# Optimization experiments

Hardware: AMD Instinct MI355X
Metric: run time of the kernel (lower is better)

Reference implementation:

```python
import jax, jax.numpy as jnp
import numpy as np
from jax import lax

PAD_IDX = 0
SOS_IDX = 1


def gru_cell(x, h, w_ih, w_hh, b_ih, b_hh):
    # PyTorch GRU cell: gates ordered [r, z, n]
    gi = x @ w_ih.T + b_ih            # [B, 3H]
    gh = h @ w_hh.T + b_hh            # [B, 3H]
    i_r, i_z, i_n = jnp.split(gi, 3, axis=-1)
    h_r, h_z, h_n = jnp.split(gh, 3, axis=-1)
    r = jax.nn.sigmoid(i_r + h_r)
    z = jax.nn.sigmoid(i_z + h_z)
    n = jnp.tanh(i_n + r * h_n)
    return (1.0 - z) * n + z * h


def setup_inputs() -> dict:
    key = jax.random.key(0)
    ks = jax.random.split(key, 24)
    B, S, T = 32, 64, 48
    Vs, Vt, E, H = 32000, 32000, 512, 1024
    sH = 1.0 / np.sqrt(H)
    sE = 1.0 / np.sqrt(E)

    def p(k, shape, scale):
        return jax.random.normal(k, shape, jnp.float32) * scale

    inp = {
        'source_ids': jax.random.randint(ks[0], (B, S), 0, Vs),
        'target_ids': jax.random.randint(ks[1], (B, T), 0, Vt),
        'enc_embed': p(ks[2], (Vs, E), 0.02).at[PAD_IDX].set(0.0),
        'enc_w_ih': p(ks[3], (3 * H, E), sE),
        'enc_w_hh': p(ks[4], (3 * H, H), sH),
        'enc_b_ih': p(ks[5], (3 * H,), sH),
        'enc_b_hh': p(ks[6], (3 * H,), sH),
        'wq': p(ks[7], (H, H), sH),
        'bq': p(ks[8], (H,), sH),
        'wk': p(ks[9], (H, H), sH),
        'bk': p(ks[10], (H,), sH),
        'ws': p(ks[11], (H,), sH),
        'bs': p(ks[12], (), sH),
        'dec_embed': p(ks[13], (Vt, E), 0.02).at[PAD_IDX].set(0.0),
        'dec_w_ih': p(ks[14], (3 * H, E + H), sH),
        'dec_w_hh': p(ks[15], (3 * H, H), sH),
        'dec_b_ih': p(ks[16], (3 * H,), sH),
        'dec_b_hh': p(ks[17], (3 * H,), sH),
        'wo': p(ks[18], (Vt, H), sH),
        'bo': p(ks[19], (Vt,), sH),
    }
    return inp


def reference(source_ids, target_ids, enc_embed, enc_w_ih, enc_w_hh, enc_b_ih,
              enc_b_hh, wq, bq, wk, bk, ws, bs, dec_embed, dec_w_ih, dec_w_hh,
              dec_b_ih, dec_b_hh, wo, bo):
    B, S = source_ids.shape
    T = target_ids.shape[1]
    H = wq.shape[0]

    # ----- encoder GRU -----
    enc_emb = enc_embed[source_ids]                  # [B,S,E] (dropout = identity, eval)
    h0 = jnp.zeros((B, H), enc_emb.dtype)

    def enc_step(h, x):
        h = gru_cell(x, h, enc_w_ih, enc_w_hh, enc_b_ih, enc_b_hh)
        return h, h

    h_final, enc_out = lax.scan(enc_step, h0, enc_emb.transpose(1, 0, 2))
    enc_out = enc_out.transpose(1, 0, 2)             # [B,S,H]

    mask = source_ids != PAD_IDX                     # [B,S]
    keys_proj = enc_out @ wk.T + bk                  # [B,S,H] (hoisted; linear, step-invariant)

    # ----- decoder with teacher forcing (ratio=1.0 => always teacher) -----
    dec_in = jnp.concatenate(
        [jnp.full((B, 1), SOS_IDX, dtype=target_ids.dtype), target_ids[:, 1:T - 1]],
        axis=1)                                      # [B,T-1]
    dec_emb = dec_embed[dec_in].transpose(1, 0, 2)   # [T-1,B,E]

    def dec_step(h, emb):
        q = h @ wq.T + bq                            # [B,H]
        scores = jnp.tanh(q[:, None, :] + keys_proj) @ ws + bs   # [B,S]
        scores = jnp.where(mask, scores, -jnp.inf)
        w = jax.nn.softmax(scores, axis=-1)          # [B,S]
        ctx = jnp.einsum('bs,bsh->bh', w, enc_out)   # [B,H]
        x = jnp.concatenate([emb, ctx], axis=-1)     # [B,E+H]
        h2 = gru_cell(x, h, dec_w_ih, dec_w_hh, dec_b_ih, dec_b_hh)
        logits = h2 @ wo.T + bo                      # [B,V]
        return h2, (logits, w)

    _, (logits, attn) = lax.scan(dec_step, h_final, dec_emb)
    logits = logits.transpose(1, 0, 2)               # [B,T-1,V]
    attn = attn.transpose(1, 0, 2)                   # [B,T-1,S]
    return logits, attn
```

## Files before the change

### kernel.cpp

```cpp
#include <hip/hip_runtime.h>


#define BB 32
#define SS 64
#define TT 48
#define TD 47
#define EE 512
#define HH 1024
#define GG 3072
#define VV 32000
#define SOS_IDX 1
#define MPAD 1536

typedef float f32x4 __attribute__((ext_vector_type(4)));
typedef short bf16x8 __attribute__((ext_vector_type(8)));

static __device__ __forceinline__ float sigmoid_f(float x) {
    return 1.0f / (1.0f + __expf(-x));
}
static __device__ __forceinline__ float tanh_f(float x) {
    return 1.0f - 2.0f / (__expf(2.0f * x) + 1.0f);
}
static __device__ __forceinline__ unsigned short f2bf(float f) {
    unsigned u = __float_as_uint(f);
    u = u + 0x7fffu + ((u >> 16) & 1u);
    return (unsigned short)(u >> 16);
}

__global__ void k_dec_idx(const int* __restrict__ tgt, int* __restrict__ idx) {
    int m = blockIdx.x * 256 + threadIdx.x;
    if (m < TD * BB) {
        int t = m >> 5, b = m & 31;
        idx[m] = (t == 0) ? SOS_IDX : tgt[b * TT + t];
    }
}

__global__ __launch_bounds__(256) void k_gemm128(
    const float* __restrict__ A, const float* __restrict__ Wt,
    const float* __restrict__ bias, float* __restrict__ C,
    const int* __restrict__ rowidx,
    int M, int N, int K, int lda, int ldw, int ldc)
{
    __shared__ __align__(16) float As[16][128];
    __shared__ __align__(16) float Bs[16][128];
    const int tid = threadIdx.x;
    const int tm = tid >> 4, tn = tid & 15;
    const int row0 = blockIdx.y * 128;
    const int col0 = blockIdx.x * 128;
    const int lr = tid >> 1;
    const int lq = tid & 1;

    long arow_off = -1;
    {
        int arow = row0 + lr;
        if (arow < M) {
            int r = rowidx ? rowidx[arow] : arow;
            arow_off = (long)r * lda;
        }
    }
    const long wrow_off = (long)(col0 + lr) * ldw;

    float acc[8][8];
#pragma unroll
    for (int i = 0; i < 8; ++i)
#pragma unroll
        for (int j = 0; j < 8; ++j) acc[i][j] = 0.f;

    for (int k0 = 0; k0 < K; k0 += 16) {
        f32x4 av0 = {0.f,0.f,0.f,0.f}, av1 = {0.f,0.f,0.f,0.f};
        if (arow_off >= 0) {
            av0 = *(const f32x4*)(A + arow_off + k0 + lq * 8);
            av1 = *(const f32x4*)(A + arow_off + k0 + lq * 8 + 4);
        }
        f32x4 wv0 = *(const f32x4*)(Wt + wrow_off + k0 + lq * 8);
        f32x4 wv1 = *(const f32x4*)(Wt + wrow_off + k0 + lq * 8 + 4);
        __syncthreads();
#pragma unroll
        for (int i = 0; i < 4; ++i) {
            As[lq * 8 + i][lr] = av0[i];
            As[lq * 8 + 4 + i][lr] = av1[i];
            Bs[lq * 8 + i][lr] = wv0[i];
            Bs[lq * 8 + 4 + i][lr] = wv1[i];
        }
        __syncthreads();
#pragma unroll
        for (int kk = 0; kk < 16; ++kk) {
            f32x4 a0 = *(const f32x4*)&As[kk][tm * 4];
            f32x4 a1 = *(const f32x4*)&As[kk][64 + tm * 4];
            f32x4 b0 = *(const f32x4*)&Bs[kk][tn * 4];
            f32x4 b1 = *(const f32x4*)&Bs[kk][64 + tn * 4];
            float a[8], b[8];
#pragma unroll
            for (int i = 0; i < 4; ++i) {
                a[i] = a0[i]; a[4 + i] = a1[i];
                b[i] = b0[i]; b[4 + i] = b1[i];
            }
#pragma unroll
            for (int i = 0; i < 8; ++i)
#pragma unroll
                for (int j = 0; j < 8; ++j) acc[i][j] += a[i] * b[j];
        }
    }

    f32x4 bv0 = {0.f,0.f,0.f,0.f}, bv1 = {0.f,0.f,0.f,0.f};
    if (bias) {
        bv0 = *(const f32x4*)(bias + col0 + tn * 4);
        bv1 = *(const f32x4*)(bias + col0 + 64 + tn * 4);
    }
#pragma unroll
    for (int i = 0; i < 8; ++i) {
        int m = row0 + ((i < 4) ? (tm * 4 + i) : (64 + tm * 4 + i - 4));
        if (m >= M) continue;
        f32x4 v0, v1;
#pragma unroll
        for (int j = 0; j < 4; ++j) {
            v0[j] = acc[i][j] + bv0[j];
            v1[j] = acc[i][4 + j] + bv1[j];
        }
        *(f32x4*)(C + (long)m * ldc + col0 + tn * 4) = v0;
        *(f32x4*)(C + (long)m * ldc + col0 + 64 + tn * 4) = v1;
    }
}

__global__ __launch_bounds__(256) void k_cvtA(
    const float* __restrict__ A, unsigned short* __restrict__ Ah,
    unsigned short* __restrict__ Al)
{
    size_t i4 = ((size_t)blockIdx.x * 256 + threadIdx.x) * 4;
    int row = (int)(i4 >> 10);
    f32x4 v = {0.f, 0.f, 0.f, 0.f};
    if (row < TD * BB) v = *(const f32x4*)(A + i4);
    ushort4 h, l;
    float hf;
    h.x = f2bf(v.x); hf = __uint_as_float((unsigned)h.x << 16); l.x = f2bf(v.x - hf);
    h.y = f2bf(v.y); hf = __uint_as_float((unsigned)h.y << 16); l.y = f2bf(v.y - hf);
    h.z = f2bf(v.z); hf = __uint_as_float((unsigned)h.z << 16); l.z = f2bf(v.z - hf);
    h.w = f2bf(v.w); hf = __uint_as_float((unsigned)h.w << 16); l.w = f2bf(v.w - hf);
    *(ushort4*)(Ah + i4) = h;
    *(ushort4*)(Al + i4) = l;
}

__global__ __launch_bounds__(256) void k_cvtB(
    const float* __restrict__ Bsrc, unsigned short* __restrict__ Bh)
{
    size_t i4 = ((size_t)blockIdx.x * 256 + threadIdx.x) * 4;
    f32x4 v = *(const f32x4*)(Bsrc + i4);
    ushort4 h;
    h.x = f2bf(v.x); h.y = f2bf(v.y); h.z = f2bf(v.z); h.w = f2bf(v.w);
    *(ushort4*)(Bh + i4) = h;
}

__global__ __launch_bounds__(256) void k_mfma_logits(
    const unsigned short* __restrict__ Ah,
    const unsigned short* __restrict__ Bh,
    const float* __restrict__ bo, float* __restrict__ C)
{
    __shared__ __align__(16) unsigned short As0[128 * 64];
    __shared__ __align__(16) unsigned short As1[128 * 64];
    __shared__ __align__(16) unsigned short Bs[128 * 64];
    const int tid = threadIdx.x;
    const int m0 = blockIdx.x * 128;
    const int n0 = blockIdx.y * 128;
    const int r = tid >> 1, half = tid & 1;
    const int lane = tid & 63, wid = tid >> 6;
    const int wm = wid >> 1, wn = wid & 1;

    f32x4 acc[4][4];
#pragma unroll
    for (int i = 0; i < 4; ++i)
#pragma unroll
        for (int j = 0; j < 4; ++j) acc[i][j] = (f32x4){0.f, 0.f, 0.f, 0.f};

    char* As0B = (char*)As0;
    char* As1B = (char*)As1;
    char* BsB  = (char*)Bs;
    const int lwb = r * 128 + half * 64;
    const int swz = (r & 7) << 4;

    for (int kt = 0; kt < 16; ++kt) {
        const int kb = kt * 64;
        const unsigned short* Ap0 = Ah + (size_t)(m0 + r) * 1024 + kb + half * 32;
        const unsigned short* Ap1 = Ap0 + (size_t)MPAD * 1024;
        const unsigned short* Bp  = Bh + (size_t)(n0 + r) * 1024 + kb + half * 32;
        f32x4 a0 = *(const f32x4*)(Ap0 + 0);
        f32x4 a1 = *(const f32x4*)(Ap0 + 8);
        f32x4 a2 = *(const f32x4*)(Ap0 + 16);
        f32x4 a3 = *(const f32x4*)(Ap0 + 24);
        f32x4 c0 = *(const f32x4*)(Ap1 + 0);
        f32x4 c1 = *(const f32x4*)(Ap1 + 8);
        f32x4 c2 = *(const f32x4*)(Ap1 + 16);
        f32x4 c3 = *(const f32x4*)(Ap1 + 24);
        f32x4 b0 = *(const f32x4*)(Bp + 0);
        f32x4 b1 = *(const f32x4*)(Bp + 8);
        f32x4 b2 = *(const f32x4*)(Bp + 16);
        f32x4 b3 = *(const f32x4*)(Bp + 24);
        __syncthreads();
        *(f32x4*)(As0B + ((lwb + 0)  ^ swz)) = a0;
        *(f32x4*)(As0B + ((lwb + 16) ^ swz)) = a1;
        *(f32x4*)(As0B + ((lwb + 32) ^ swz)) = a2;
        *(f32x4*)(As0B + ((lwb + 48) ^ swz)) = a3;
        *(f32x4*)(As1B + ((lwb + 0)  ^ swz)) = c0;
        *(f32x4*)(As1B + ((lwb + 16) ^ swz)) = c1;
        *(f32x4*)(As1B + ((lwb + 32) ^ swz)) = c2;
        *(f32x4*)(As1B + ((lwb + 48) ^ swz)) = c3;
        *(f32x4*)(BsB  + ((lwb + 0)  ^ swz)) = b0;
        *(f32x4*)(BsB  + ((lwb + 16) ^ swz)) = b1;
        *(f32x4*)(BsB  + ((lwb + 32) ^ swz)) = b2;
        *(f32x4*)(BsB  + ((lwb + 48) ^ swz)) = b3;
        __syncthreads();
#pragma unroll
        for (int ks = 0; ks < 2; ++ks) {
            bf16x8 bf[4], af[4], ag[4];
#pragma unroll
            for (int u = 0; u < 4; ++u) {
                int nl = wn * 64 + u * 16 + (lane & 15);
                int byteB = nl * 128 + ks * 64 + ((lane >> 4) << 4);
                bf[u] = *(const bf16x8*)(BsB + (byteB ^ ((nl & 7) << 4)));
                int ml = wm * 64 + u * 16 + (lane & 15);
                int byteA = ml * 128 + ks * 64 + ((lane >> 4) << 4);
                af[u] = *(const bf16x8*)(As0B + (byteA ^ ((ml & 7) << 4)));
                ag[u] = *(const bf16x8*)(As1B + (byteA ^ ((ml & 7) << 4)));
            }
#pragma unroll
            for (int mi = 0; mi < 4; ++mi)
#pragma unroll
                for (int ni = 0; ni < 4; ++ni) {
                    acc[mi][ni] = __builtin_amdgcn_mfma_f32_16x16x32_bf16(
                        af[mi], bf[ni], acc[mi][ni], 0, 0, 0);
                    acc[mi][ni] = __builtin_amdgcn_mfma_f32_16x16x32_bf16(
                        ag[mi], bf[ni], acc[mi][ni], 0, 0, 0);
                }
        }
    }

    const int cl = lane & 15, rq = lane >> 4;
#pragma unroll
    for (int ni = 0; ni < 4; ++ni) {
        int col = n0 + wn * 64 + ni * 16 + cl;
        float bias = bo[col];
#pragma unroll
        for (int mi = 0; mi < 4; ++mi) {
#pragma unroll
            for (int j = 0; j < 4; ++j) {
                int m = m0 + wm * 64 + mi * 16 + rq * 4 + j;
                if (m < TD * BB) {
                    int orow = (m & 31) * TD + (m >> 5);
                    C[(size_t)orow * VV + col] = acc[mi][ni][j] + bias;
                }
            }
        }
    }
}

__global__ __launch_bounds__(512, 2) void k_enc_step(
    const float* __restrict__ gi, const float* __restrict__ Whh,
    const float* __restrict__ bhh, float* __restrict__ enc_out, int s)
{
    __shared__ float red[12][16][32];
    __shared__ float sums[12][32];
    const int tid = threadIdx.x, bid = blockIdx.x;
    const int b = tid & 31, ks = tid >> 5;
    const int j0 = bid * 4;
    const int kc = ks * 64;

    float acc[12];
#pragma unroll
    for (int u = 0; u < 12; ++u) acc[u] = 0.f;
    if (s > 0) {
        f32x4 hreg[16];
        const float* hb = enc_out + ((size_t)b * SS + (s - 1)) * HH + kc;
#pragma unroll
        for (int i = 0; i < 16; ++i) hreg[i] = *(const f32x4*)(hb + (i << 2));
#pragma unroll
        for (int jj = 0; jj < 4; ++jj) {
            const float* pr = Whh + ((size_t)(j0 + jj) << 10) + kc;
            const float* pz = Whh + ((size_t)(HH + j0 + jj) << 10) + kc;
            const float* pn = Whh + ((size_t)(2 * HH + j0 + jj) << 10) + kc;
            float ar = 0.f, az = 0.f, an = 0.f;
#pragma unroll
            for (int i = 0; i < 16; ++i) {
                f32x4 h4 = hreg[i];
                f32x4 w;
                w = *(const f32x4*)(pr + (i << 2));
                ar += h4.x * w.x + h4.y * w.y + h4.z * w.z + h4.w * w.w;
                w = *(const f32x4*)(pz + (i << 2));
                az += h4.x * w.x + h4.y * w.y + h4.z * w.z + h4.w * w.w;
                w = *(const f32x4*)(pn + (i << 2));
                an += h4.x * w.x + h4.y * w.y + h4.z * w.z + h4.w * w.w;
            }
            acc[jj] = ar; acc[4 + jj] = az; acc[8 + jj] = an;
        }
    }
#pragma unroll
    for (int u = 0; u < 12; ++u) red[u][ks][b] = acc[u];
    __syncthreads();
    if (tid < 384) {
        int u = tid >> 5, fb = tid & 31;
        float x = 0.f;
#pragma unroll
        for (int q = 0; q < 16; ++q) x += red[u][q][fb];
        sums[u][fb] = x;
    }
    __syncthreads();
    if (tid < 32) {
        const f32x4 bh0 = *(const f32x4*)(bhh + j0);
        const f32x4 bh1 = *(const f32x4*)(bhh + HH + j0);
        const f32x4 bh2 = *(const f32x4*)(bhh + 2 * HH + j0);
        const float* gr = gi + (size_t)(tid * SS + s) * GG;
        f32x4 g0 = *(const f32x4*)(gr + j0);
        f32x4 g1 = *(const f32x4*)(gr + HH + j0);
        f32x4 g2 = *(const f32x4*)(gr + 2 * HH + j0);
        f32x4 hold = {0.f, 0.f, 0.f, 0.f};
        if (s > 0) hold = *(const f32x4*)(enc_out + ((size_t)tid * SS + (s - 1)) * HH + j0);
        f32x4 hn;
#pragma unroll
        for (int e = 0; e < 4; ++e) {
            float r = sigmoid_f(g0[e] + sums[e][tid] + bh0[e]);
            float z = sigmoid_f(g1[e] + sums[4 + e][tid] + bh1[e]);
            float n = tanh_f(g2[e] + r * (sums[8 + e][tid] + bh2[e]));
            hn[e] = (1.f - z) * n + z * hold[e];
        }
        *(f32x4*)(enc_out + ((size_t)tid * SS + s) * HH + j0) = hn;
    }
}

__global__ __launch_bounds__(512, 2) void k_hq(
    const float* __restrict__ hbase, long hstride,
    const float* __restrict__ Whh, const float* __restrict__ wq,
    const float* __restrict__ bq, float* __restrict__ qbuf,
    float* __restrict__ hsums)
{
    __shared__ float red[16][16][32];
    __shared__ float qsum[4][32];
    const int tid = threadIdx.x, bid = blockIdx.x;
    const int b = tid & 31, ks = tid >> 5;
    const int j0 = bid * 4;
    const int kc = ks * 64;

    f32x4 hreg[16];
    const float* hb = hbase + (size_t)b * hstride + kc;
#pragma unroll
    for (int i = 0; i < 16; ++i) hreg[i] = *(const f32x4*)(hb + (i << 2));
    float acc[16];
#pragma unroll
    for (int jj = 0; jj < 4; ++jj) {
        const float* pr = Whh + ((size_t)(j0 + jj) << 10) + kc;
        const float* pz = Whh + ((size_t)(HH + j0 + jj) << 10) + kc;
        const float* pn = Whh + ((size_t)(2 * HH + j0 + jj) << 10) + kc;
        const float* pq = wq + ((size_t)(j0 + jj) << 10) + kc;
        float ar = 0.f, az = 0.f, an = 0.f, aq = 0.f;
#pragma unroll
        for (int i = 0; i < 16; ++i) {
            f32x4 h4 = hreg[i];
            f32x4 w;
            w = *(const f32x4*)(pr + (i << 2));
            ar += h4.x * w.x + h4.y * w.y + h4.z * w.z + h4.w * w.w;
            w = *(const f32x4*)(pz + (i << 2));
            az += h4.x * w.x + h4.y * w.y + h4.z * w.z + h4.w * w.w;
            w = *(const f32x4*)(pn + (i << 2));
            an += h4.x * w.x + h4.y * w.y + h4.z * w.z + h4.w * w.w;
            w = *(const f32x4*)(pq + (i << 2));
            aq += h4.x * w.x + h4.y * w.y + h4.z * w.z + h4.w * w.w;
        }
        acc[jj] = ar; acc[4 + jj] = az; acc[8 + jj] = an; acc[12 + jj] = aq;
    }
#pragma unroll
    for (int u = 0; u < 16; ++u) red[u][ks][b] = acc[u];
    __syncthreads();
    {
        int u = tid >> 5, fb = tid & 31;
        float x = 0.f;
#pragma unroll
        for (int q = 0; q < 16; ++q) x += red[u][q][fb];
        if (u < 12) {
            int g = u >> 2, jj = u & 3;
            hsums[(size_t)g * BB * HH + (size_t)fb * HH + j0 + jj] = x;
        } else {
            qsum[u - 12][fb] = x;
        }
    }
    __syncthreads();
    if (tid < 32) {
        const f32x4 bq4 = *(const f32x4*)(bq + j0);
        f32x4 qv;
        qv.x = qsum[0][tid] + bq4.x;
        qv.y = qsum[1][tid] + bq4.y;
        qv.z = qsum[2][tid] + bq4.z;
        qv.w = qsum[3][tid] + bq4.w;
        *(f32x4*)(qbuf + (size_t)tid * HH + j0) = qv;
    }
}

__global__ __launch_bounds__(512, 2) void k_attn_fin(
    const float* __restrict__ qbuf, const float* __restrict__ keys,
    const float* __restrict__ wsv, const float* __restrict__ bsv,
    const int* __restrict__ src, const float* __restrict__ encproj,
    const float* __restrict__ gi, const float* __restrict__ bhh,
    const float* __restrict__ hsums, const float* __restrict__ hbase,
    long hstride, float* __restrict__ h2all, float* __restrict__ attn_out,
    int t)
{
    __shared__ float qs[HH];
    __shared__ float wss[HH];
    __shared__ float sc[8][64];
    __shared__ float wl[64];
    __shared__ float xls[3 * 512];
    const int ab = blockIdx.x & 31, part = blockIdx.x >> 5;
    const int tid = threadIdx.x;
    if (tid < 256) {
        *(f32x4*)&qs[tid * 4] = *(const f32x4*)(qbuf + (size_t)ab * HH + tid * 4);
        *(f32x4*)&wss[tid * 4] = *(const f32x4*)(wsv + tid * 4);
    }
    __syncthreads();
    {
        const int s4 = tid >> 3, kq = tid & 7;
        const float* kr = keys + (size_t)(ab * SS + s4) * HH + kq * 128;
        float a = 0.f;
        for (int i = 0; i < 32; ++i) {
            f32x4 kv = *(const f32x4*)(kr + (i << 2));
            int k = kq * 128 + (i << 2);
            a += tanh_f(qs[k] + kv.x) * wss[k]
               + tanh_f(qs[k + 1] + kv.y) * wss[k + 1]
               + tanh_f(qs[k + 2] + kv.z) * wss[k + 2]
               + tanh_f(qs[k + 3] + kv.w) * wss[k + 3];
        }
        sc[kq][s4] = a;
    }
    __syncthreads();
    if (tid < 64) {
        float v = bsv[0];
#pragma unroll
        for (int q = 0; q < 8; ++q) v += sc[q][tid];
        bool valid = src[ab * SS + tid] != 0;
        float m = valid ? v : -3.0e38f;
        for (int off = 32; off; off >>= 1) m = fmaxf(m, __shfl_xor(m, off));
        float e = valid ? __expf(v - m) : 0.f;
        float ssum = e;
        for (int off = 32; off; off >>= 1) ssum += __shfl_xor(ssum, off);
        float wgt = e / ssum;
        wl[tid] = wgt;
        if (part == 0)
            attn_out[((size_t)ab * TD + t) * SS + tid] = wgt;
    }
    __syncthreads();
    {
        float xa[3] = {0.f, 0.f, 0.f};
        const int colbase = part * 512 + tid;
        for (int s2 = 0; s2 < SS; ++s2) {
            float wgt = wl[s2];
            const float* ep = encproj + (size_t)(ab * SS + s2) * GG + colbase;
#pragma unroll
            for (int u = 0; u < 3; ++u)
                xa[u] += wgt * ep[u * HH];
        }
#pragma unroll
        for (int u = 0; u < 3; ++u) xls[u * 512 + tid] = xa[u];
    }
    __syncthreads();
    {
        const int j = part * 512 + tid;
        const float* gr = gi + (size_t)(t * BB + ab) * GG;
        float g0 = gr[j] + xls[tid];
        float g1 = gr[HH + j] + xls[512 + tid];
        float g2 = gr[2 * HH + j] + xls[1024 + tid];
        float sh0 = hsums[(size_t)0 * BB * HH + (size_t)ab * HH + j];
        float sh1 = hsums[(size_t)1 * BB * HH + (size_t)ab * HH + j];
        float sh2 = hsums[(size_t)2 * BB * HH + (size_t)ab * HH + j];
        float r = sigmoid_f(g0 + sh0 + bhh[j]);
        float z = sigmoid_f(g1 + sh1 + bhh[HH + j]);
        float n = tanh_f(g2 + r * (sh2 + bhh[2 * HH + j]));
        float hold = hbase[(size_t)ab * hstride + j];
        h2all[((size_t)t * BB + ab) * HH + j] = (1.f - z) * n + z * hold;
    }
}

extern "C" void kernel_launch(void* const* d_in, const int* in_sizes, int n_in,
                              void* d_out, int out_size, void* d_ws, size_t ws_size,
                              hipStream_t stream)
{
    const int*   src  = (const int*)d_in[0];
    const int*   tgt  = (const int*)d_in[1];
    const float* eemb = (const float*)d_in[2];
    const float* ewih = (const float*)d_in[3];
    const float* ewhh = (const float*)d_in[4];
    const float* ebih = (const float*)d_in[5];
    const float* ebhh = (const float*)d_in[6];
    const float* wq   = (const float*)d_in[7];
    const float* bq   = (const float*)d_in[8];
    const float* wk   = (const float*)d_in[9];
    const float* bk   = (const float*)d_in[10];
    const float* wsv  = (const float*)d_in[11];
    const float* bsv  = (const float*)d_in[12];
    const float* demb = (const float*)d_in[13];
    const float* dwih = (const float*)d_in[14];
    const float* dwhh = (const float*)d_in[15];
    const float* dbih = (const float*)d_in[16];
    const float* dbhh = (const float*)d_in[17];
    const float* wo   = (const float*)d_in[18];
    const float* bo   = (const float*)d_in[19];
    float* out = (float*)d_out;

    float* w = (float*)d_ws;
    float* enc_gi  = w;
    float* dec_gi  = enc_gi  + (size_t)BB * SS * GG;
    float* enc_out = dec_gi  + (size_t)TD * BB * GG;
    float* keys    = enc_out + (size_t)BB * SS * HH;
    float* h2all   = keys    + (size_t)BB * SS * HH;
    float* qbuf    = h2all   + (size_t)TD * BB * HH;
    float* hsums   = qbuf    + (size_t)BB * HH;
    int*   didx    = (int*)(hsums + (size_t)3 * BB * HH);
    unsigned short* Ah = (unsigned short*)(didx + TD * BB + 32);
    unsigned short* Al = Ah + (size_t)MPAD * 1024;
    unsigned short* Bh = (unsigned short*)w;

    float* encproj = enc_gi;
    float* attn_out = out + (size_t)BB * TD * VV;

    k_dec_idx<<<dim3((TD * BB + 255) / 256), 256, 0, stream>>>(tgt, didx);

    k_gemm128<<<dim3(GG / 128, (BB * SS) / 128), 256, 0, stream>>>(
        eemb, ewih, ebih, enc_gi, src, BB * SS, GG, EE, EE, EE, GG);
    k_gemm128<<<dim3(GG / 128, (TD * BB + 127) / 128), 256, 0, stream>>>(
        demb, dwih, dbih, dec_gi, didx, TD * BB, GG, EE, EE, EE + HH, GG);

    for (int s = 0; s < SS; ++s)
        k_enc_step<<<dim3(256), dim3(512), 0, stream>>>(
            enc_gi, ewhh, ebhh, enc_out, s);

    k_gemm128<<<dim3(HH / 128, (BB * SS) / 128), 256, 0, stream>>>(
        enc_out, wk, bk, keys, nullptr, BB * SS, HH, HH, HH, HH, HH);
    k_gemm128<<<dim3(GG / 128, (BB * SS) / 128), 256, 0, stream>>>(
        enc_out, dwih + EE, nullptr, encproj, nullptr,
        BB * SS, GG, HH, HH, EE + HH, GG);

    for (int t = 0; t < TD; ++t) {
        const float* hbase = (t == 0) ? enc_out + (size_t)(SS - 1) * HH
                                      : h2all + (size_t)(t - 1) * BB * HH;
        long hstride = (t == 0) ? (long)SS * HH : (long)HH;
        k_hq<<<dim3(256), dim3(512), 0, stream>>>(
            hbase, hstride, dwhh, wq, bq, qbuf, hsums);
        k_attn_fin<<<dim3(64), dim3(512), 0, stream>>>(
            qbuf, keys, wsv, bsv, src, encproj, dec_gi, dbhh, hsums,
            hbase, hstride, h2all, attn_out, t);
    }

    k_cvtA<<<dim3(MPAD * 1024 / 1024), 256, 0, stream>>>(h2all, Ah, Al);
    k_cvtB<<<dim3(VV * 1024 / 1024), 256, 0, stream>>>(wo, Bh);
    k_mfma_logits<<<dim3(MPAD / 128, VV / 128), 256, 0, stream>>>(
        Ah, Bh, bo, out);
}
```

Before: 3.984 ms.

## Transpose encoder context projection and split attention finalize across more blocks

```diff
diff --git a/kernel.cpp b/kernel.cpp
--- a/kernel.cpp
+++ b/kernel.cpp
@@ -39,7 +39,7 @@
     const float* __restrict__ A, const float* __restrict__ Wt,
     const float* __restrict__ bias, float* __restrict__ C,
     const int* __restrict__ rowidx,
-    int M, int N, int K, int lda, int ldw, int ldc)
+    int M, int N, int K, int lda, int ldw, int ldc, int tmode)
 {
     __shared__ __align__(16) float As[16][128];
     __shared__ __align__(16) float Bs[16][128];
@@ -106,6 +106,21 @@
     if (bias) {
         bv0 = *(const f32x4*)(bias + col0 + tn * 4);
         bv1 = *(const f32x4*)(bias + col0 + 64 + tn * 4);
+    }
+    if (tmode == 1) {
+#pragma unroll
+        for (int i = 0; i < 8; ++i) {
+            int m = row0 + ((i < 4) ? (tm * 4 + i) : (64 + tm * 4 + i - 4));
+            if (m >= M) continue;
+            int b = m >> 6, s = m & 63;
+            float* base = C + ((size_t)b * GG) * 64 + s;
+#pragma unroll
+            for (int j = 0; j < 4; ++j) {
+                base[(size_t)(col0 + tn * 4 + j) * 64] = acc[i][j] + bv0[j];
+                base[(size_t)(col0 + 64 + tn * 4 + j) * 64] = acc[i][4 + j] + bv1[j];
+            }
+        }
+        return;
     }
 #pragma unroll
     for (int i = 0; i < 8; ++i) {
@@ -394,7 +409,7 @@
 __global__ __launch_bounds__(512, 2) void k_attn_fin(
     const float* __restrict__ qbuf, const float* __restrict__ keys,
     const float* __restrict__ wsv, const float* __restrict__ bsv,
-    const int* __restrict__ src, const float* __restrict__ encproj,
+    const int* __restrict__ src, const float* __restrict__ encprojT,
     const float* __restrict__ gi, const float* __restrict__ bhh,
     const float* __restrict__ hsums, const float* __restrict__ hbase,
     long hstride, float* __restrict__ h2all, float* __restrict__ attn_out,
@@ -404,7 +419,7 @@
     __shared__ float wss[HH];
     __shared__ float sc[8][64];
     __shared__ float wl[64];
-    __shared__ float xls[3 * 512];
+    __shared__ float xls[384];
     const int ab = blockIdx.x & 31, part = blockIdx.x >> 5;
     const int tid = threadIdx.x;
     if (tid < 256) {
@@ -443,26 +458,26 @@
             attn_out[((size_t)ab * TD + t) * SS + tid] = wgt;
     }
     __syncthreads();
-    {
-        float xa[3] = {0.f, 0.f, 0.f};
-        const int colbase = part * 512 + tid;
-        for (int s2 = 0; s2 < SS; ++s2) {
-            float wgt = wl[s2];
-            const float* ep = encproj + (size_t)(ab * SS + s2) * GG + colbase;
-#pragma unroll
-            for (int u = 0; u < 3; ++u)
-                xa[u] += wgt * ep[u * HH];
-        }
-#pragma unroll
-        for (int u = 0; u < 3; ++u) xls[u * 512 + tid] = xa[u];
-    }
-    __syncthreads();
-    {
-        const int j = part * 512 + tid;
+    if (tid < 384) {
+        const int g = tid >> 7, jj = tid & 127;
+        const int col = (g << 10) + (part << 7) + jj;
+        const float* ep = encprojT + ((size_t)ab * GG + col) * 64;
+        float xa = 0.f;
+#pragma unroll
+        for (int i = 0; i < 16; ++i) {
+            f32x4 v = *(const f32x4*)(ep + (i << 2));
+            xa += wl[i * 4 + 0] * v.x + wl[i * 4 + 1] * v.y
+                + wl[i * 4 + 2] * v.z + wl[i * 4 + 3] * v.w;
+        }
+        xls[tid] = xa;
+    }
+    __syncthreads();
+    if (tid < 128) {
+        const int j = (part << 7) + tid;
         const float* gr = gi + (size_t)(t * BB + ab) * GG;
         float g0 = gr[j] + xls[tid];
-        float g1 = gr[HH + j] + xls[512 + tid];
-        float g2 = gr[2 * HH + j] + xls[1024 + tid];
+        float g1 = gr[HH + j] + xls[128 + tid];
+        float g2 = gr[2 * HH + j] + xls[256 + tid];
         float sh0 = hsums[(size_t)0 * BB * HH + (size_t)ab * HH + j];
         float sh1 = hsums[(size_t)1 * BB * HH + (size_t)ab * HH + j];
         float sh2 = hsums[(size_t)2 * BB * HH + (size_t)ab * HH + j];
@@ -513,25 +528,25 @@
     unsigned short* Al = Ah + (size_t)MPAD * 1024;
     unsigned short* Bh = (unsigned short*)w;
 
-    float* encproj = enc_gi;
+    float* encprojT = enc_gi;
     float* attn_out = out + (size_t)BB * TD * VV;
 
     k_dec_idx<<<dim3((TD * BB + 255) / 256), 256, 0, stream>>>(tgt, didx);
 
     k_gemm128<<<dim3(GG / 128, (BB * SS) / 128), 256, 0, stream>>>(
-        eemb, ewih, ebih, enc_gi, src, BB * SS, GG, EE, EE, EE, GG);
+        eemb, ewih, ebih, enc_gi, src, BB * SS, GG, EE, EE, EE, GG, 0);
     k_gemm128<<<dim3(GG / 128, (TD * BB + 127) / 128), 256, 0, stream>>>(
-        demb, dwih, dbih, dec_gi, didx, TD * BB, GG, EE, EE, EE + HH, GG);
+        demb, dwih, dbih, dec_gi, didx, TD * BB, GG, EE, EE, EE + HH, GG, 0);
 
     for (int s = 0; s < SS; ++s)
         k_enc_step<<<dim3(256), dim3(512), 0, stream>>>(
             enc_gi, ewhh, ebhh, enc_out, s);
 
     k_gemm128<<<dim3(HH / 128, (BB * SS) / 128), 256, 0, stream>>>(
-        enc_out, wk, bk, keys, nullptr, BB * SS, HH, HH, HH, HH, HH);
+        enc_out, wk, bk, keys, nullptr, BB * SS, HH, HH, HH, HH, HH, 0);
     k_gemm128<<<dim3(GG / 128, (BB * SS) / 128), 256, 0, stream>>>(
-        enc_out, dwih + EE, nullptr, encproj, nullptr,
-        BB * SS, GG, HH, HH, EE + HH, GG);
+        enc_out, dwih + EE, nullptr, encprojT, nullptr,
+        BB * SS, GG, HH, HH, EE + HH, GG, 1);
 
     for (int t = 0; t < TD; ++t) {
         const float* hbase = (t == 0) ? enc_out + (size_t)(SS - 1) * HH
@@ -539,8 +554,8 @@
         long hstride = (t == 0) ? (long)SS * HH : (long)HH;
         k_hq<<<dim3(256), dim3(512), 0, stream>>>(
             hbase, hstride, dwhh, wq, bq, qbuf, hsums);
-        k_attn_fin<<<dim3(64), dim3(512), 0, stream>>>(
-            qbuf, keys, wsv, bsv, src, encproj, dec_gi, dbhh, hsums,
+        k_attn_fin<<<dim3(256), dim3(512), 0, stream>>>(
+            qbuf, keys, wsv, bsv, src, encprojT, dec_gi, dbhh, hsums,
             hbase, hstride, h2all, attn_out, t);
     }
 
```

Result: no change. 4.048 ms (+1.6%).
